# Optimization experiments

Measured on AMD Instinct MI355X. Metric: run time of the kernel, lower is better.

The kernel has to match this reference:

```python
import jax, jax.numpy as jnp
import numpy as np

D_IN = 1024
D_OUT = 1024
BATCH = 4
SEQ = 2048


def setup_inputs() -> dict:
    key = jax.random.key(0)
    kx, kq, kk, kv = jax.random.split(key, 4)
    # nn.Linear default init: U(-1/sqrt(d_in), 1/sqrt(d_in)); exact dist irrelevant for a reference
    bound = 1.0 / np.sqrt(D_IN)
    x = jax.random.normal(kx, (BATCH, SEQ, D_IN), dtype=jnp.float32)
    W_query = jax.random.uniform(kq, (D_IN, D_OUT), dtype=jnp.float32, minval=-bound, maxval=bound)
    W_key = jax.random.uniform(kk, (D_IN, D_OUT), dtype=jnp.float32, minval=-bound, maxval=bound)
    W_value = jax.random.uniform(kv, (D_IN, D_OUT), dtype=jnp.float32, minval=-bound, maxval=bound)
    return {"x": x, "W_query": W_query, "W_key": W_key, "W_value": W_value}


def reference(x, W_query, W_key, W_value):
    # x: [b, s, d_in]; projections (qkv_bias=False)
    q = jnp.einsum("bsd,df->bsf", x, W_query)  # [b, s, d_out]
    k = jnp.einsum("bsd,df->bsf", x, W_key)
    v = jnp.einsum("bsd,df->bsf", x, W_value)

    scale = 1.0 / jnp.sqrt(jnp.asarray(k.shape[-1], dtype=x.dtype))
    scores = jnp.einsum("bqf,bkf->bqk", q, k) * scale  # [b, s, s]

    s = x.shape[1]
    causal = jnp.tril(jnp.ones((s, s), dtype=bool))  # True where allowed
    scores = jnp.where(causal[None, :, :], scores, -jnp.inf)

    weights = jax.nn.softmax(scores, axis=-1)
    # dropout_ratio=0.0 -> identity
    return jnp.einsum("bqk,bkf->bqf", weights, v)  # [b, s, d_out]
```

## Files before the change

kernel.cpp:

```cpp
#include <hip/hip_runtime.h>


typedef __bf16 bf16x8 __attribute__((ext_vector_type(8)));
typedef float f32x4 __attribute__((ext_vector_type(4)));

__device__ __forceinline__ unsigned short f2bf(float f) {
  unsigned int u = __builtin_bit_cast(unsigned int, f);
  u += 0x7FFFu + ((u >> 16) & 1u);
  return (unsigned short)(u >> 16);
}
__device__ __forceinline__ float bf2f(unsigned short h) {
  unsigned int u = ((unsigned int)h) << 16;
  return __builtin_bit_cast(float, u);
}

#define GLDS16(g, l)                                                                   \
  __builtin_amdgcn_global_load_lds((const __attribute__((address_space(1))) void*)(g), \
                                   (__attribute__((address_space(3))) void*)(l), 16, 0, 0)

__global__ __launch_bounds__(256) void k_cvt(const float* __restrict__ in,
                                             unsigned short* __restrict__ out, long n) {
  long i = ((long)blockIdx.x * 256 + threadIdx.x) * 8;
  if (i >= n) return;
  float4 a = *(const float4*)(in + i);
  float4 b = *(const float4*)(in + i + 4);
  uint4 o;
  o.x = (unsigned)f2bf(a.x) | ((unsigned)f2bf(a.y) << 16);
  o.y = (unsigned)f2bf(a.z) | ((unsigned)f2bf(a.w) << 16);
  o.z = (unsigned)f2bf(b.x) | ((unsigned)f2bf(b.y) << 16);
  o.w = (unsigned)f2bf(b.z) | ((unsigned)f2bf(b.w) << 16);
  *(uint4*)(out + i) = o;
}

__global__ void k_trans_w(const float* __restrict__ W0, const float* __restrict__ W1,
                          const float* __restrict__ W2, unsigned short* __restrict__ Wt, int D) {
  const float* W = blockIdx.z == 0 ? W0 : (blockIdx.z == 1 ? W1 : W2);
  unsigned short* out = Wt + (long)blockIdx.z * D * D;
  __shared__ float tile[32][33];
  int tx = threadIdx.x, ty = threadIdx.y;
  int bx = blockIdx.x * 32, by = blockIdx.y * 32;
#pragma unroll
  for (int j = 0; j < 4; ++j) tile[ty + j * 8][tx] = W[(long)(by + ty + j * 8) * D + bx + tx];
  __syncthreads();
#pragma unroll
  for (int j = 0; j < 4; ++j)
    out[(long)(bx + ty + j * 8) * D + by + tx] = f2bf(tile[tx][ty + j * 8]);
}

template <typename CT, int MODE>
__global__ __launch_bounds__(256) void k_gemm_bt(const unsigned short* __restrict__ A,
                                                 const unsigned short* __restrict__ B,
                                                 CT* __restrict__ C, int nx, int ny, int N, int K,
                                                 long sA, long sB, long sC, float alpha) {
  const unsigned bid = blockIdx.x;
  const unsigned cpx = gridDim.x >> 3;
  const unsigned logical = (bid & 7) * cpx + (bid >> 3);
  int z, by, bx;
  if constexpr (MODE == 1) {
    const int per_z = ny * (ny + 1) / 2;
    z = (int)(logical / per_z);
    int r = (int)(logical - (unsigned)z * per_z);
    int b = (int)((sqrtf(8.f * (float)r + 1.f) - 1.f) * 0.5f);
    while ((b + 1) * (b + 2) / 2 <= r) ++b;
    while (b * (b + 1) / 2 > r) --b;
    by = b;
    bx = r - b * (b + 1) / 2;
  } else {
    const int per_z = nx * ny;
    z = (int)(logical / per_z);
    int r = (int)(logical - (unsigned)z * per_z);
    int j = r / nx;
    bx = r - j * nx;
    by = (MODE == 2) ? ((j & 1) ? (ny - 1 - (j >> 1)) : (j >> 1)) : j;
  }
  const int m0 = by * 128;
  const int n0 = bx * 128;
  A += (long)z * sA;
  B += (long)z * sB;
  C += (long)z * sC;

  __shared__ unsigned short As[128 * 64];
  __shared__ unsigned short Bs[128 * 64];
  char* const AsB = (char*)As;
  char* const BsB = (char*)Bs;

  const int t = threadIdx.x;
  const int l = t & 63;
  const int w = t >> 6;
  const int wr = (w >> 1) * 64;
  const int wc = (w & 1) * 64;

  const int srow = t >> 3;
  const int sch = (t & 7) ^ (srow & 7);
  const unsigned short* Ag = A + (long)(m0 + srow) * K + sch * 8;
  const unsigned short* Bg = B + (long)(n0 + srow) * K + sch * 8;
  const int soff = t * 16;

  const int ar = wr + (l & 15);
  const int brr = wc + (l & 15);
  const int kc = l >> 4;

  f32x4 acc[4][4];
#pragma unroll
  for (int i = 0; i < 4; ++i)
#pragma unroll
    for (int j = 0; j < 4; ++j) acc[i][j] = f32x4{0.f, 0.f, 0.f, 0.f};

  int KT = K >> 6;
  if (MODE == 2) {
    int kt2 = (m0 + 128) >> 6;
    KT = KT < kt2 ? KT : kt2;
  }

  for (int kt = 0; kt < KT; ++kt) {
    const long ko = (long)kt * 64;
#pragma unroll
    for (int i = 0; i < 4; ++i) GLDS16(Ag + (long)i * 32 * K + ko, AsB + i * 4096 + soff);
#pragma unroll
    for (int i = 0; i < 4; ++i) GLDS16(Bg + (long)i * 32 * K + ko, BsB + i * 4096 + soff);
    __syncthreads();
#pragma unroll
    for (int kk = 0; kk < 2; ++kk) {
      bf16x8 av[4], bv[4];
#pragma unroll
      for (int m = 0; m < 4; ++m) {
        int r = ar + m * 16;
        int c = (kk * 4 + kc) ^ (r & 7);
        av[m] = *(const bf16x8*)(AsB + r * 128 + c * 16);
      }
#pragma unroll
      for (int n = 0; n < 4; ++n) {
        int r = brr + n * 16;
        int c = (kk * 4 + kc) ^ (r & 7);
        bv[n] = *(const bf16x8*)(BsB + r * 128 + c * 16);
      }
#pragma unroll
      for (int m = 0; m < 4; ++m)
#pragma unroll
        for (int n = 0; n < 4; ++n)
          acc[m][n] = __builtin_amdgcn_mfma_f32_16x16x32_bf16(av[m], bv[n], acc[m][n], 0, 0, 0);
    }
    __syncthreads();
  }

  const int rb = m0 + wr + (l >> 4) * 4;
  const int cb = n0 + wc + (l & 15);
#pragma unroll
  for (int m = 0; m < 4; ++m)
#pragma unroll
    for (int n = 0; n < 4; ++n)
#pragma unroll
      for (int i = 0; i < 4; ++i) {
        float v = acc[m][n][i] * alpha;
        long off = (long)(rb + m * 16 + i) * N + (cb + n * 16);
        if constexpr (sizeof(CT) == 2)
          C[off] = f2bf(v);
        else
          C[off] = v;
      }
}

__global__ __launch_bounds__(256) void k_softmax(unsigned short* __restrict__ P, int S) {
  const int t = threadIdx.x;
  const int wv = t >> 6, l = t & 63;
  const int q = blockIdx.x * 4 + wv;
  unsigned short* row = P + ((long)blockIdx.y * S + q) * S;

  uint4 raw[4];
#pragma unroll
  for (int j = 0; j < 4; ++j) raw[j] = ((const uint4*)row)[j * 64 + l];
  float v[32];
#pragma unroll
  for (int j = 0; j < 4; ++j) {
    unsigned int rw[4] = {raw[j].x, raw[j].y, raw[j].z, raw[j].w};
#pragma unroll
    for (int e = 0; e < 8; ++e)
      v[j * 8 + e] = bf2f((unsigned short)((rw[e >> 1] >> ((e & 1) * 16)) & 0xFFFF));
  }

  float mx = -3.0e38f;
#pragma unroll
  for (int j = 0; j < 4; ++j)
#pragma unroll
    for (int e = 0; e < 8; ++e) {
      int col = j * 512 + l * 8 + e;
      if (col <= q) mx = fmaxf(mx, v[j * 8 + e]);
    }
#pragma unroll
  for (int o = 32; o >= 1; o >>= 1) mx = fmaxf(mx, __shfl_xor(mx, o, 64));

  float s = 0.f;
#pragma unroll
  for (int j = 0; j < 4; ++j)
#pragma unroll
    for (int e = 0; e < 8; ++e) {
      int col = j * 512 + l * 8 + e;
      float ev = (col <= q) ? __expf(v[j * 8 + e] - mx) : 0.f;
      v[j * 8 + e] = ev;
      s += ev;
    }
#pragma unroll
  for (int o = 32; o >= 1; o >>= 1) s += __shfl_xor(s, o, 64);
  const float inv = 1.f / s;

#pragma unroll
  for (int j = 0; j < 4; ++j) {
    uint4 ow;
    unsigned int o2[4];
#pragma unroll
    for (int jj = 0; jj < 4; ++jj)
      o2[jj] = (unsigned)f2bf(v[j * 8 + 2 * jj] * inv) |
               ((unsigned)f2bf(v[j * 8 + 2 * jj + 1] * inv) << 16);
    ow.x = o2[0]; ow.y = o2[1]; ow.z = o2[2]; ow.w = o2[3];
    ((uint4*)row)[j * 64 + l] = ow;
  }
}

extern "C" void kernel_launch(void* const* d_in, const int* in_sizes, int n_in, void* d_out,
                              int out_size, void* d_ws, size_t ws_size, hipStream_t stream) {
  const int B = 4, S = 2048, D = 1024;
  const long MS = (long)B * S;

  const float* x = (const float*)d_in[0];
  const float* Wq = (const float*)d_in[1];
  const float* Wk = (const float*)d_in[2];
  const float* Wv = (const float*)d_in[3];
  float* out = (float*)d_out;

  unsigned short* xb = (unsigned short*)d_ws;
  unsigned short* Wt = xb + MS * D;
  unsigned short* Qb = Wt + 3L * D * D;
  unsigned short* Kb = Qb + MS * D;
  unsigned short* Vt = Kb + MS * D;
  unsigned short* P  = Vt + MS * D;
  (void)ws_size;

  long n = MS * D;
  k_cvt<<<dim3((unsigned)(n / 8 / 256)), 256, 0, stream>>>(x, xb, n);
  k_trans_w<<<dim3(32, 32, 3), dim3(32, 8), 0, stream>>>(Wq, Wk, Wv, Wt, D);
  k_gemm_bt<unsigned short, 0><<<1024, 256, 0, stream>>>(
      xb, Wt, Qb, D / 128, (int)(MS / 128), D, D,
      0L, (long)D * D, MS * D, 1.0f);
  k_gemm_bt<unsigned short, 0><<<512, 256, 0, stream>>>(
      Wt + 2L * D * D, xb, Vt, S / 128, D / 128, S, D,
      0L, (long)S * D, (long)D * S, 1.0f);
  k_gemm_bt<unsigned short, 1><<<544, 256, 0, stream>>>(
      Qb, Kb, P, S / 128, S / 128, S, D,
      (long)S * D, (long)S * D, (long)S * S, 0.03125f);
  k_softmax<<<dim3(S / 4, B), 256, 0, stream>>>(P, S);
  k_gemm_bt<float, 2><<<512, 256, 0, stream>>>(
      P, Vt, out, D / 128, S / 128, D, S,
      (long)S * S, (long)D * S, (long)S * D, 1.0f);
}
```

Measured before the change: 163.8 us.

## Add 256x256 pipelined GEMM for Q/K projection and skip masked softmax chunks

Introduces a 512-thread 256x256-tile GEMM with double-buffered LDS staging, interleaved global-to-LDS loads and MFMA phases, explicit vmcnt waits and setprio, and uses it for the fused Q/K projection. The softmax kernel now loads and processes only the 512-column chunks that can contain unmasked entries for each causal row. The goal is more reuse per tile and better overlap of loads with MFMA work in the projection, plus less softmax memory traffic. The cost is higher register and LDS pressure (128KB LDS per block), which may limit occupancy, and fewer workgroups in the grid.

```diff
diff --git a/kernel.cpp b/kernel.cpp
--- a/kernel.cpp
+++ b/kernel.cpp
@@ -45,6 +45,154 @@
 #pragma unroll
   for (int j = 0; j < 4; ++j)
     out[(long)(bx + ty + j * 8) * D + by + tx] = f2bf(tile[tx][ty + j * 8]);
+}
+
+template <typename CT>
+__global__ __launch_bounds__(512, 2) void k_gemm256(const unsigned short* __restrict__ A,
+                                                    const unsigned short* __restrict__ B,
+                                                    CT* __restrict__ C, int nx, int ny, int N,
+                                                    int K, long sA, long sB, long sC,
+                                                    float alpha) {
+  const unsigned bid = blockIdx.x;
+  const unsigned cpx = gridDim.x >> 3;
+  const unsigned logical = (bid & 7) * cpx + (bid >> 3);
+  const int per_z = nx * ny;
+  const int z = (int)(logical / per_z);
+  const int rem = (int)(logical - (unsigned)z * per_z);
+  const int by = rem / nx;
+  const int bx = rem - by * nx;
+  const int m0 = by * 256, n0 = bx * 256;
+  A += (long)z * sA;
+  B += (long)z * sB;
+  C += (long)z * sC;
+
+  __shared__ char lds[131072];
+
+  const int t = threadIdx.x;
+  const int l = t & 63;
+  const int w = t >> 6;
+  const int wm = w >> 2;
+  const int wn = w & 3;
+
+  const int srow = t >> 3;
+  const int sch = (t & 7) ^ (srow & 7);
+  const int soff = t * 16;
+
+#define STG(mat, bf, hf, kt)                                                              \
+  do {                                                                                    \
+    const unsigned short* g =                                                             \
+        ((mat) ? B + (long)(n0 + (hf)*128 + srow) * K : A + (long)(m0 + (hf)*128 + srow) * K) + \
+        (long)(kt)*64 + sch * 8;                                                          \
+    char* d = lds + (mat)*65536 + (bf)*32768 + (hf)*16384 + soff;                         \
+    GLDS16(g, d);                                                                         \
+    GLDS16(g + (long)64 * K, d + 8192);                                                   \
+  } while (0)
+
+  const int lx = l & 15;
+  const int kx0 = ((l >> 4) ^ (l & 7)) * 16;
+  const int kx1 = ((4 + (l >> 4)) ^ (l & 7)) * 16;
+  char* const aB = lds + wm * 16384 + lx * 128;
+  char* const bB = lds + 65536 + (wn >> 1) * 16384 + ((wn & 1) * 64 + lx) * 128;
+
+  bf16x8 av[4][2], bv0[2][2], bv1[2][2];
+  f32x4 acc[8][4];
+#pragma unroll
+  for (int i = 0; i < 8; ++i)
+#pragma unroll
+    for (int jn = 0; jn < 4; ++jn) acc[i][jn] = f32x4{0.f, 0.f, 0.f, 0.f};
+
+#define RDA(bf, mh)                                                     \
+  do {                                                                  \
+    _Pragma("unroll") for (int m4 = 0; m4 < 4; ++m4) {                  \
+      char* p = aB + (bf)*32768 + ((mh)*64 + m4 * 16) * 128;            \
+      av[m4][0] = *(const bf16x8*)(p + kx0);                            \
+      av[m4][1] = *(const bf16x8*)(p + kx1);                            \
+    }                                                                   \
+  } while (0)
+#define RDB(dst, bf, nh)                                                \
+  do {                                                                  \
+    _Pragma("unroll") for (int n2 = 0; n2 < 2; ++n2) {                  \
+      char* p = bB + (bf)*32768 + (((nh)*2 + n2) * 16) * 128;           \
+      dst[n2][0] = *(const bf16x8*)(p + kx0);                           \
+      dst[n2][1] = *(const bf16x8*)(p + kx1);                           \
+    }                                                                   \
+  } while (0)
+#define MFM(bv, mh, nh)                                                                    \
+  do {                                                                                     \
+    __builtin_amdgcn_s_setprio(1);                                                         \
+    _Pragma("unroll") for (int m4 = 0; m4 < 4; ++m4) _Pragma("unroll") for (int n2 = 0;    \
+                                                                            n2 < 2; ++n2) { \
+      acc[(mh)*4 + m4][(nh)*2 + n2] = __builtin_amdgcn_mfma_f32_16x16x32_bf16(             \
+          av[m4][0], bv[n2][0], acc[(mh)*4 + m4][(nh)*2 + n2], 0, 0, 0);                   \
+      acc[(mh)*4 + m4][(nh)*2 + n2] = __builtin_amdgcn_mfma_f32_16x16x32_bf16(             \
+          av[m4][1], bv[n2][1], acc[(mh)*4 + m4][(nh)*2 + n2], 0, 0, 0);                   \
+    }                                                                                      \
+    __builtin_amdgcn_s_setprio(0);                                                         \
+  } while (0)
+#define BAR __builtin_amdgcn_s_barrier()
+#define VMC(n) asm volatile("s_waitcnt vmcnt(" #n ")" ::: "memory")
+
+  const int KT = K >> 6;
+  const int NIT = KT >> 1;
+
+  STG(0, 0, 0, 0); STG(0, 0, 1, 0); STG(1, 0, 0, 0); STG(1, 0, 1, 0);
+  STG(1, 1, 0, 1); STG(1, 1, 1, 1); STG(0, 1, 0, 1);
+  VMC(6);
+  BAR;
+
+  for (int j = 0; j < NIT; ++j) {
+    const bool full = (j < NIT - 1);
+    RDA(0, 0); RDB(bv0, 0, 0);
+    STG(0, 1, 1, 2 * j + 1);
+    BAR; MFM(bv0, 0, 0); BAR;
+    RDB(bv1, 0, 1);
+    BAR; MFM(bv1, 0, 1); BAR;
+    RDA(0, 1);
+    if (full) STG(1, 0, 0, 2 * j + 2);
+    BAR; MFM(bv1, 1, 1); BAR;
+    if (full) {
+      STG(0, 0, 0, 2 * j + 2); STG(1, 0, 1, 2 * j + 2);
+      VMC(6);
+    } else {
+      VMC(0);
+    }
+    BAR; MFM(bv0, 1, 0); BAR;
+    RDA(1, 0); RDB(bv0, 1, 0);
+    if (full) STG(0, 0, 1, 2 * j + 2);
+    BAR; MFM(bv0, 0, 0); BAR;
+    RDB(bv1, 1, 1);
+    BAR; MFM(bv1, 0, 1); BAR;
+    RDA(1, 1);
+    if (full) STG(1, 1, 0, 2 * j + 3);
+    BAR; MFM(bv1, 1, 1); BAR;
+    if (full) {
+      STG(1, 1, 1, 2 * j + 3); STG(0, 1, 0, 2 * j + 3);
+      VMC(6);
+    }
+    BAR; MFM(bv0, 1, 0); BAR;
+  }
+
+  const int rb = m0 + wm * 128 + (l >> 4) * 4;
+  const int cb = n0 + wn * 64 + (l & 15);
+#pragma unroll
+  for (int m = 0; m < 8; ++m)
+#pragma unroll
+    for (int n = 0; n < 4; ++n)
+#pragma unroll
+      for (int i = 0; i < 4; ++i) {
+        float v = acc[m][n][i] * alpha;
+        long off = (long)(rb + m * 16 + i) * N + (cb + n * 16);
+        if constexpr (sizeof(CT) == 2)
+          C[off] = f2bf(v);
+        else
+          C[off] = v;
+      }
+#undef STG
+#undef RDA
+#undef RDB
+#undef MFM
+#undef BAR
+#undef VMC
 }
 
 template <typename CT, int MODE>
@@ -165,26 +313,32 @@
   const int wv = t >> 6, l = t & 63;
   const int q = blockIdx.x * 4 + wv;
   unsigned short* row = P + ((long)blockIdx.y * S + q) * S;
+  const int nch = (q >> 9) + 1;
 
   uint4 raw[4];
-#pragma unroll
-  for (int j = 0; j < 4; ++j) raw[j] = ((const uint4*)row)[j * 64 + l];
   float v[32];
 #pragma unroll
+  for (int j = 0; j < 4; ++j)
+    if (j < nch) raw[j] = ((const uint4*)row)[j * 64 + l];
+#pragma unroll
   for (int j = 0; j < 4; ++j) {
-    unsigned int rw[4] = {raw[j].x, raw[j].y, raw[j].z, raw[j].w};
-#pragma unroll
-    for (int e = 0; e < 8; ++e)
-      v[j * 8 + e] = bf2f((unsigned short)((rw[e >> 1] >> ((e & 1) * 16)) & 0xFFFF));
+    if (j < nch) {
+      unsigned int rw[4] = {raw[j].x, raw[j].y, raw[j].z, raw[j].w};
+#pragma unroll
+      for (int e = 0; e < 8; ++e)
+        v[j * 8 + e] = bf2f((unsigned short)((rw[e >> 1] >> ((e & 1) * 16)) & 0xFFFF));
+    }
   }
 
   float mx = -3.0e38f;
 #pragma unroll
   for (int j = 0; j < 4; ++j)
-#pragma unroll
-    for (int e = 0; e < 8; ++e) {
-      int col = j * 512 + l * 8 + e;
-      if (col <= q) mx = fmaxf(mx, v[j * 8 + e]);
+    if (j < nch) {
+#pragma unroll
+      for (int e = 0; e < 8; ++e) {
+        int col = j * 512 + l * 8 + e;
+        if (col <= q) mx = fmaxf(mx, v[j * 8 + e]);
+      }
     }
 #pragma unroll
   for (int o = 32; o >= 1; o >>= 1) mx = fmaxf(mx, __shfl_xor(mx, o, 64));
@@ -192,28 +346,31 @@
   float s = 0.f;
 #pragma unroll
   for (int j = 0; j < 4; ++j)
-#pragma unroll
-    for (int e = 0; e < 8; ++e) {
-      int col = j * 512 + l * 8 + e;
-      float ev = (col <= q) ? __expf(v[j * 8 + e] - mx) : 0.f;
-      v[j * 8 + e] = ev;
-      s += ev;
+    if (j < nch) {
+#pragma unroll
+      for (int e = 0; e < 8; ++e) {
+        int col = j * 512 + l * 8 + e;
+        float ev = (col <= q) ? __expf(v[j * 8 + e] - mx) : 0.f;
+        v[j * 8 + e] = ev;
+        s += ev;
+      }
     }
 #pragma unroll
   for (int o = 32; o >= 1; o >>= 1) s += __shfl_xor(s, o, 64);
   const float inv = 1.f / s;
 
 #pragma unroll
-  for (int j = 0; j < 4; ++j) {
-    uint4 ow;
-    unsigned int o2[4];
-#pragma unroll
-    for (int jj = 0; jj < 4; ++jj)
-      o2[jj] = (unsigned)f2bf(v[j * 8 + 2 * jj] * inv) |
-               ((unsigned)f2bf(v[j * 8 + 2 * jj + 1] * inv) << 16);
-    ow.x = o2[0]; ow.y = o2[1]; ow.z = o2[2]; ow.w = o2[3];
-    ((uint4*)row)[j * 64 + l] = ow;
-  }
+  for (int j = 0; j < 4; ++j)
+    if (j < nch) {
+      uint4 ow;
+      unsigned int o2[4];
+#pragma unroll
+      for (int jj = 0; jj < 4; ++jj)
+        o2[jj] = (unsigned)f2bf(v[j * 8 + 2 * jj] * inv) |
+                 ((unsigned)f2bf(v[j * 8 + 2 * jj + 1] * inv) << 16);
+      ow.x = o2[0]; ow.y = o2[1]; ow.z = o2[2]; ow.w = o2[3];
+      ((uint4*)row)[j * 64 + l] = ow;
+    }
 }
 
 extern "C" void kernel_launch(void* const* d_in, const int* in_sizes, int n_in, void* d_out,
@@ -238,8 +395,8 @@
   long n = MS * D;
   k_cvt<<<dim3((unsigned)(n / 8 / 256)), 256, 0, stream>>>(x, xb, n);
   k_trans_w<<<dim3(32, 32, 3), dim3(32, 8), 0, stream>>>(Wq, Wk, Wv, Wt, D);
-  k_gemm_bt<unsigned short, 0><<<1024, 256, 0, stream>>>(
-      xb, Wt, Qb, D / 128, (int)(MS / 128), D, D,
+  k_gemm256<unsigned short><<<256, 512, 0, stream>>>(
+      xb, Wt, Qb, D / 256, (int)(MS / 256), D, D,
       0L, (long)D * D, MS * D, 1.0f);
   k_gemm_bt<unsigned short, 0><<<512, 256, 0, stream>>>(
       Wt + 2L * D * D, xb, Vt, S / 128, D / 128, S, D,
```

After: 153.5 us. 6.3% less time.
